# Kernel optimization log

Hardware: AMD Instinct MI355X
Metric: run time of the kernel (lower is better)

## Reference

```python
import jax, jax.numpy as jnp
import numpy as np

EPS_NORM = 1e-12  # torch F.normalize eps
EPS_LOG = 1e-8


def setup_inputs() -> dict:
    key = jax.random.key(0)
    target_prob = jax.random.uniform(key, (65536, 1024), dtype=jnp.float32)
    return {"target_prob": target_prob}


def reference(target_prob) -> jnp.ndarray:
    # F.normalize(x, dim=0): L2-normalize each column, norm clamped at eps
    norm = jnp.sqrt(jnp.sum(target_prob * target_prob, axis=0, keepdims=True))
    p = target_prob / jnp.maximum(norm, EPS_NORM)
    # per-row entropy: -sum_j p * log(p + 1e-8)
    row_entropy = -jnp.sum(p * jnp.log(p + EPS_LOG), axis=1)
    return jnp.mean(row_entropy)
```

## Files before the change

kernel.cpp:

```cpp
#include <hip/hip_runtime.h>
#include <hip/hip_bf16.h>


#define ROWS  65536
#define COLS  1024
#define C4    (COLS / 4)
#define GRID  2048
#define ITERS (ROWS / GRID)
#define NSLOT 64

#define EPS_NORM 1e-12f

#define WS_PART   0
#define WS_BPART  (NSLOT * 3 * COLS)

__global__ __launch_bounds__(256) void fused_stats_kernel(
    const float* __restrict__ x, float* __restrict__ part) {
    const int t = threadIdx.x;
    const float4* xr = reinterpret_cast<const float4*>(x)
                     + (size_t)blockIdx.x * C4 + t;

    float4 s1 = make_float4(0.f, 0.f, 0.f, 0.f);
    float4 s2 = make_float4(0.f, 0.f, 0.f, 0.f);
    float4 s3 = make_float4(0.f, 0.f, 0.f, 0.f);
    #pragma unroll 4
    for (int k = 0; k < ITERS; ++k) {
        float4 v = xr[(size_t)k * GRID * C4];
        s1.x += v.x; s1.y += v.y; s1.z += v.z; s1.w += v.w;
        s2.x = fmaf(v.x, v.x, s2.x);
        s2.y = fmaf(v.y, v.y, s2.y);
        s2.z = fmaf(v.z, v.z, s2.z);
        s2.w = fmaf(v.w, v.w, s2.w);
        s3.x += (v.x > 0.f) ? v.x * __logf(v.x) : 0.f;
        s3.y += (v.y > 0.f) ? v.y * __logf(v.y) : 0.f;
        s3.z += (v.z > 0.f) ? v.z * __logf(v.z) : 0.f;
        s3.w += (v.w > 0.f) ? v.w * __logf(v.w) : 0.f;
    }

    float* dst = part + (size_t)(blockIdx.x & (NSLOT - 1)) * 3 * COLS + 4 * t;
    atomicAdd(dst + 0,            s1.x);
    atomicAdd(dst + 1,            s1.y);
    atomicAdd(dst + 2,            s1.z);
    atomicAdd(dst + 3,            s1.w);
    atomicAdd(dst + COLS + 0,     s2.x);
    atomicAdd(dst + COLS + 1,     s2.y);
    atomicAdd(dst + COLS + 2,     s2.z);
    atomicAdd(dst + COLS + 3,     s2.w);
    atomicAdd(dst + 2 * COLS + 0, s3.x);
    atomicAdd(dst + 2 * COLS + 1, s3.y);
    atomicAdd(dst + 2 * COLS + 2, s3.z);
    atomicAdd(dst + 2 * COLS + 3, s3.w);
}

__global__ __launch_bounds__(256) void finalize_kernel(
    const float* __restrict__ part, float* __restrict__ bpart) {
    const int t = threadIdx.x;
    const int j = blockIdx.x * 256 + t;
    float a1 = 0.f, a2 = 0.f, a3 = 0.f;
    #pragma unroll 8
    for (int r = 0; r < NSLOT; ++r) {
        const float* p = part + (size_t)r * 3 * COLS + j;
        a1 += p[0];
        a2 += p[COLS];
        a3 += p[2 * COLS];
    }
    float n = fmaxf(sqrtf(a2), EPS_NORM);
    float contrib = (a3 - __logf(n) * a1) / n;

    #pragma unroll
    for (int o = 32; o > 0; o >>= 1) contrib += __shfl_down(contrib, o, 64);

    __shared__ float wsum[4];
    if ((t & 63) == 0) wsum[t >> 6] = contrib;
    __syncthreads();
    if (t == 0) bpart[blockIdx.x] = wsum[0] + wsum[1] + wsum[2] + wsum[3];
}

__global__ __launch_bounds__(64) void final_reduce_kernel(
    const float* __restrict__ bpart, float* __restrict__ out) {
    const int t = threadIdx.x;
    float a = (t < 4) ? bpart[t] : 0.f;
    #pragma unroll
    for (int o = 32; o > 0; o >>= 1) a += __shfl_down(a, o, 64);
    if (t == 0) out[0] = -a * (1.0f / (float)ROWS);
}

extern "C" void kernel_launch(void* const* d_in, const int* in_sizes, int n_in,
                              void* d_out, int out_size, void* d_ws, size_t ws_size,
                              hipStream_t stream) {
    const float* x = (const float*)d_in[0];
    float* out = (float*)d_out;
    float* ws = (float*)d_ws;
    float* part  = ws + WS_PART;
    float* bpart = ws + WS_BPART;

    hipMemsetAsync(part, 0, (size_t)NSLOT * 3 * COLS * sizeof(float), stream);

    fused_stats_kernel<<<GRID, 256, 0, stream>>>(x, part);
    finalize_kernel<<<COLS / 256, 256, 0, stream>>>(part, bpart);
    final_reduce_kernel<<<1, 64, 0, stream>>>(bpart, out);
}
```

Measured before the change: 404.7 us.

## Replace atomic slot accumulation with per-block partial stores and a tree reduction

```diff
diff --git a/kernel.cpp b/kernel.cpp
--- a/kernel.cpp
+++ b/kernel.cpp
@@ -7,12 +7,12 @@
 #define C4    (COLS / 4)
 #define GRID  2048
 #define ITERS (ROWS / GRID)
-#define NSLOT 64
+#define RED1  64
 
 #define EPS_NORM 1e-12f
 
-#define WS_PART   0
-#define WS_BPART  (NSLOT * 3 * COLS)
+#define WS_TMP   (GRID * 3 * COLS)
+#define WS_BPART (WS_TMP + RED1 * 3 * COLS)
 
 __global__ __launch_bounds__(256) void fused_stats_kernel(
     const float* __restrict__ x, float* __restrict__ part) {
@@ -23,7 +23,7 @@
     float4 s1 = make_float4(0.f, 0.f, 0.f, 0.f);
     float4 s2 = make_float4(0.f, 0.f, 0.f, 0.f);
     float4 s3 = make_float4(0.f, 0.f, 0.f, 0.f);
-    #pragma unroll 4
+    #pragma unroll 8
     for (int k = 0; k < ITERS; ++k) {
         float4 v = xr[(size_t)k * GRID * C4];
         s1.x += v.x; s1.y += v.y; s1.z += v.z; s1.w += v.w;
@@ -37,29 +37,43 @@
         s3.w += (v.w > 0.f) ? v.w * __logf(v.w) : 0.f;
     }
 
-    float* dst = part + (size_t)(blockIdx.x & (NSLOT - 1)) * 3 * COLS + 4 * t;
-    atomicAdd(dst + 0,            s1.x);
-    atomicAdd(dst + 1,            s1.y);
-    atomicAdd(dst + 2,            s1.z);
-    atomicAdd(dst + 3,            s1.w);
-    atomicAdd(dst + COLS + 0,     s2.x);
-    atomicAdd(dst + COLS + 1,     s2.y);
-    atomicAdd(dst + COLS + 2,     s2.z);
-    atomicAdd(dst + COLS + 3,     s2.w);
-    atomicAdd(dst + 2 * COLS + 0, s3.x);
-    atomicAdd(dst + 2 * COLS + 1, s3.y);
-    atomicAdd(dst + 2 * COLS + 2, s3.z);
-    atomicAdd(dst + 2 * COLS + 3, s3.w);
+    float4* dst = reinterpret_cast<float4*>(part + (size_t)blockIdx.x * 3 * COLS) + t;
+    dst[0]      = s1;
+    dst[C4]     = s2;
+    dst[2 * C4] = s3;
+}
+
+__global__ __launch_bounds__(256) void reduce1_kernel(
+    const float* __restrict__ part, float* __restrict__ tmp) {
+    const int t = threadIdx.x;
+    const float4* p = reinterpret_cast<const float4*>(
+        part + (size_t)blockIdx.x * (GRID / RED1) * 3 * COLS) + t;
+
+    float4 a1 = make_float4(0.f, 0.f, 0.f, 0.f);
+    float4 a2 = make_float4(0.f, 0.f, 0.f, 0.f);
+    float4 a3 = make_float4(0.f, 0.f, 0.f, 0.f);
+    #pragma unroll 4
+    for (int s = 0; s < GRID / RED1; ++s) {
+        const float4* ps = p + (size_t)s * 3 * C4;
+        float4 v1 = ps[0], v2 = ps[C4], v3 = ps[2 * C4];
+        a1.x += v1.x; a1.y += v1.y; a1.z += v1.z; a1.w += v1.w;
+        a2.x += v2.x; a2.y += v2.y; a2.z += v2.z; a2.w += v2.w;
+        a3.x += v3.x; a3.y += v3.y; a3.z += v3.z; a3.w += v3.w;
+    }
+    float4* d = reinterpret_cast<float4*>(tmp + (size_t)blockIdx.x * 3 * COLS) + t;
+    d[0]      = a1;
+    d[C4]     = a2;
+    d[2 * C4] = a3;
 }
 
 __global__ __launch_bounds__(256) void finalize_kernel(
-    const float* __restrict__ part, float* __restrict__ bpart) {
+    const float* __restrict__ tmp, float* __restrict__ bpart) {
     const int t = threadIdx.x;
     const int j = blockIdx.x * 256 + t;
     float a1 = 0.f, a2 = 0.f, a3 = 0.f;
     #pragma unroll 8
-    for (int r = 0; r < NSLOT; ++r) {
-        const float* p = part + (size_t)r * 3 * COLS + j;
+    for (int r = 0; r < RED1; ++r) {
+        const float* p = tmp + (size_t)r * 3 * COLS + j;
         a1 += p[0];
         a2 += p[COLS];
         a3 += p[2 * COLS];
@@ -91,12 +105,12 @@
     const float* x = (const float*)d_in[0];
     float* out = (float*)d_out;
     float* ws = (float*)d_ws;
-    float* part  = ws + WS_PART;
+    float* part  = ws;
+    float* tmp   = ws + WS_TMP;
     float* bpart = ws + WS_BPART;
 
-    hipMemsetAsync(part, 0, (size_t)NSLOT * 3 * COLS * sizeof(float), stream);
-
     fused_stats_kernel<<<GRID, 256, 0, stream>>>(x, part);
-    finalize_kernel<<<COLS / 256, 256, 0, stream>>>(part, bpart);
+    reduce1_kernel<<<RED1, 256, 0, stream>>>(part, tmp);
+    finalize_kernel<<<COLS / 256, 256, 0, stream>>>(tmp, bpart);
     final_reduce_kernel<<<1, 64, 0, stream>>>(bpart, out);
 }
```

Measured after the change: 382.0 us. 1.06x faster.
